# Kernel optimization log

Measured on AMD Instinct MI355X. Metric: run time of the kernel, lower is better.

## Reference

```python
import jax, jax.numpy as jnp
import numpy as np
from jax.ops import segment_sum

N_NODES = 50000
N_EDGES = 50000
N_GRAPHS = 1024


def _inv_deg(idx, num_segments):
    deg = segment_sum(jnp.ones(idx.shape[0], jnp.float32), idx, num_segments=num_segments)
    return jnp.where(deg > 0, 1.0 / deg, 0.0)


def hypergraph_conv(x, W, b, node_idx, edge_idx):
    # PyG HypergraphConv (use_attention=False, heads=1, hyperedge_weight=1):
    # out = D^{-1} H B^{-1} H^T (X W) + b
    D = _inv_deg(node_idx, N_NODES)   # inverse node degree [N]
    B = _inv_deg(edge_idx, N_EDGES)   # inverse hyperedge degree [E]
    xl = x @ W                         # [N, out]
    # node -> hyperedge aggregation
    edge_feat = B[:, None] * segment_sum(xl[node_idx], edge_idx, num_segments=N_EDGES)
    # hyperedge -> node aggregation
    out = D[:, None] * segment_sum(edge_feat[edge_idx], node_idx, num_segments=N_NODES)
    return out + b


def global_mean_pool(x, batch):
    s = segment_sum(x, batch, num_segments=N_GRAPHS)
    cnt = segment_sum(jnp.ones(x.shape[0], jnp.float32), batch, num_segments=N_GRAPHS)
    return s / jnp.maximum(cnt, 1.0)[:, None]


def setup_inputs() -> dict:
    key = jax.random.key(0)
    ks = jax.random.split(key, 16)
    F, H = 128, 256
    def lin(k, fi, fo):
        s = 1.0 / np.sqrt(fi)
        k1, k2 = jax.random.split(k)
        return (jax.random.uniform(k1, (fi, fo), jnp.float32, -s, s),
                jax.random.uniform(k2, (fo,), jnp.float32, -s, s))
    W1, b1 = lin(ks[0], F, H)
    W2, b2 = lin(ks[1], H, 2 * H)
    W3, b3 = lin(ks[2], 2 * H, H)
    Wl1, bl1 = lin(ks[3], H, H // 2)
    Wl2, bl2 = lin(ks[4], H // 2, 1)
    x = jax.random.normal(ks[5], (N_NODES, F), jnp.float32)
    hyperedge_index = jax.random.randint(ks[6], (2, 400000), 0, N_EDGES, jnp.int64)
    batch = jnp.sort(jax.random.randint(ks[7], (N_NODES,), 0, N_GRAPHS, jnp.int64))
    return {"x": x, "hyperedge_index": hyperedge_index, "batch": batch,
            "W1": W1, "b1": b1, "W2": W2, "b2": b2, "W3": W3, "b3": b3,
            "Wl1": Wl1, "bl1": bl1, "Wl2": Wl2, "bl2": bl2}


def reference(x, hyperedge_index, batch, W1, b1, W2, b2, W3, b3, Wl1, bl1, Wl2, bl2):
    node_idx, edge_idx = hyperedge_index[0], hyperedge_index[1]
    h = jax.nn.relu(hypergraph_conv(x, W1, b1, node_idx, edge_idx))
    h = jax.nn.relu(hypergraph_conv(h, W2, b2, node_idx, edge_idx))
    h = jax.nn.relu(hypergraph_conv(h, W3, b3, node_idx, edge_idx))
    g = global_mean_pool(h, batch)              # [G, H]
    g = jax.nn.relu(g @ Wl1 + bl1)
    out = g @ Wl2 + bl2                          # [G, 1]
    return out
```

## Files before the change

### kernel.cpp

```cpp
#include <hip/hip_runtime.h>
#include <hip/hip_bf16.h>

#define N_NODES  50000
#define N_EDGES  50000
#define N_INC    400000
#define N_GRAPHS 1024
#define M_PAD    50048
#define SEG_CAP  50176

typedef __bf16 bf16x8 __attribute__((ext_vector_type(8)));
typedef float  f32x4  __attribute__((ext_vector_type(4)));

__device__ __forceinline__ unsigned short f2bf(float f) {
    __hip_bfloat16 h = __float2bfloat16(f);
    return __builtin_bit_cast(unsigned short, h);
}
__device__ __forceinline__ float bflo(unsigned int u) {
    return __builtin_bit_cast(float, u << 16);
}
__device__ __forceinline__ float bfhi(unsigned int u) {
    return __builtin_bit_cast(float, u & 0xffff0000u);
}
__device__ __forceinline__ unsigned int packbf(float a, float b) {
    return (unsigned int)f2bf(a) | ((unsigned int)f2bf(b) << 16);
}
__device__ __forceinline__ void load_lds16(const unsigned short* g, unsigned short* l) {
    __builtin_amdgcn_global_load_lds((const __attribute__((address_space(1))) void*)g,
                                     (__attribute__((address_space(3))) void*)l, 16, 0, 0);
}

#define NB_INC  1563
#define NB_CONV 6250
#define NB_W1   128
#define NB_W2   512
#define NB_W3   512
__global__ __launch_bounds__(256) void normhist_kernel(const int* __restrict__ hei,
                                                       int* __restrict__ nidx, int* __restrict__ eidx,
                                                       unsigned short* __restrict__ rn,
                                                       unsigned short* __restrict__ re,
                                                       int* __restrict__ ndeg_p, int* __restrict__ edeg_p,
                                                       const float* __restrict__ x,
                                                       unsigned short* __restrict__ xbf,
                                                       const float* __restrict__ W1, unsigned short* __restrict__ wt1,
                                                       const float* __restrict__ W2, unsigned short* __restrict__ wt2,
                                                       const float* __restrict__ W3, unsigned short* __restrict__ wt3) {
    int b = blockIdx.x, t = threadIdx.x;
    if (b < NB_INC) {
        __shared__ int s32;
        if (t == 0) s32 = 0;
        __syncthreads();
        int probe = hei[4 * t + 1] | hei[4 * t + 3];
        if (probe) s32 = 1;
        __syncthreads();
        int is32 = s32;
        int i = b * 256 + t;
        if (i < N_INC) {
            int n, e;
            if (is32) { n = hei[i];     e = hei[N_INC + i]; }
            else      { n = hei[2 * i]; e = hei[2 * N_INC + 2 * i]; }
            nidx[i] = n; eidx[i] = e;
            rn[i] = (unsigned short)atomicAdd(&ndeg_p[n << 4], 1);
            re[i] = (unsigned short)atomicAdd(&edeg_p[e << 4], 1);
        }
    } else if (b < NB_INC + NB_CONV) {
        int i = (b - NB_INC) * 256 + t;
        float4 v = *(const float4*)(x + 4 * (size_t)i);
        ushort4 o;
        o.x = f2bf(v.x); o.y = f2bf(v.y); o.z = f2bf(v.z); o.w = f2bf(v.w);
        *(ushort4*)(xbf + 4 * (size_t)i) = o;
    } else if (b < NB_INC + NB_CONV + NB_W1) {
        int i = (b - NB_INC - NB_CONV) * 256 + t;
        int k = i >> 8, n = i & 255;
        wt1[n * 128 + k] = f2bf(W1[i]);
    } else if (b < NB_INC + NB_CONV + NB_W1 + NB_W2) {
        int i = (b - NB_INC - NB_CONV - NB_W1) * 256 + t;
        int k = i >> 9, n = i & 511;
        wt2[n * 256 + k] = f2bf(W2[i]);
    } else {
        int i = (b - NB_INC - NB_CONV - NB_W1 - NB_W2) * 256 + t;
        int k = i >> 8, n = i & 255;
        wt3[n * 512 + k] = f2bf(W3[i]);
    }
}

__global__ __launch_bounds__(256) void scan_up_f(const int* __restrict__ edeg_p,
                                                 const int* __restrict__ ndeg_p,
                                                 const int* __restrict__ hei,
                                                 const int* __restrict__ braw,
                                                 int* __restrict__ eoff, int* __restrict__ noff,
                                                 int* __restrict__ goff,
                                                 int* __restrict__ partials) {
    int b = blockIdx.x, t = threadIdx.x;
    if (b >= 98) {
        __shared__ int s32;
        if (t == 0) s32 = 0;
        __syncthreads();
        int probe = hei[4 * t + 1] | hei[4 * t + 3];
        if (probe) s32 = 1;
        __syncthreads();
        int is32 = s32;
        int g = (b - 98) * 256 + t;
        int lo = 0, hi = N_NODES;
        while (lo < hi) {
            int mid = (lo + hi) >> 1;
            int v = is32 ? braw[mid] : braw[2 * mid];
            if (v < g) lo = mid + 1; else hi = mid;
        }
        goff[g] = lo;
        if (g == 1023) goff[1024] = N_NODES;
        return;
    }
    __shared__ int lds[256];
    const int* in; int* outp; int lb;
    if (b < 49) { in = edeg_p; outp = eoff; lb = b; }
    else        { in = ndeg_p; outp = noff; lb = b - 49; }
    int base = lb * 1024 + t * 4;
    int4 v;
    v.x = in[(size_t)(base + 0) << 4];
    v.y = in[(size_t)(base + 1) << 4];
    v.z = in[(size_t)(base + 2) << 4];
    v.w = in[(size_t)(base + 3) << 4];
    int s = v.x + v.y + v.z + v.w;
    lds[t] = s;
    __syncthreads();
    for (int off = 1; off < 256; off <<= 1) {
        int u = (t >= off) ? lds[t - off] : 0;
        __syncthreads();
        lds[t] += u;
        __syncthreads();
    }
    int excl = lds[t] - s;
    if (t == 255) partials[b] = lds[255];
    int4 o;
    o.x = excl;
    o.y = excl + v.x;
    o.z = o.y + v.y;
    o.w = o.z + v.z;
    *(int4*)(outp + base) = o;
}

__global__ __launch_bounds__(256) void scan_down_f(int* __restrict__ eoff,
                                                   int* __restrict__ noff,
                                                   const int* __restrict__ partials) {
    __shared__ int lds[98];
    int b = blockIdx.x, t = threadIdx.x;
    if (t < 98) lds[t] = partials[t];
    __syncthreads();
    if (t < 2) {
        int lo = t * 49, hi = lo + 49;
        int run = 0;
        for (int i = lo; i < hi; ++i) { int x = lds[i]; lds[i] = run; run += x; }
    }
    __syncthreads();
    int* outp; int lb;
    if (b < 49) { outp = eoff; lb = b; }
    else        { outp = noff; lb = b - 49; }
    int base = lb * 1024 + t * 4;
    int p = lds[b];
    int4 v = *(const int4*)(outp + base);
    v.x += p; v.y += p; v.z += p; v.w += p;
    *(int4*)(outp + base) = v;
}

__global__ __launch_bounds__(256) void prep_kernel(const int* __restrict__ nidx,
                                                   const int* __restrict__ eidx,
                                                   const unsigned short* __restrict__ rn,
                                                   const unsigned short* __restrict__ re,
                                                   const int* __restrict__ eoff,
                                                   const int* __restrict__ noff,
                                                   unsigned short* __restrict__ csre,
                                                   unsigned short* __restrict__ csrn) {
    int i = blockIdx.x * 256 + threadIdx.x;
    if (i >= N_INC) return;
    int n = nidx[i], e = eidx[i];
    csre[eoff[e] + re[i]] = (unsigned short)n;
    csrn[noff[n] + rn[i]] = (unsigned short)e;
}

template <bool EPI>
__global__ __launch_bounds__(256) void gemm128_kernel(const unsigned short* __restrict__ A,
                                                      const unsigned short* __restrict__ Bt,
                                                      const float* __restrict__ bias,
                                                      unsigned short* __restrict__ C,
                                                      int M, int K, int N) {
    __shared__ unsigned short As[128 * 32];
    __shared__ unsigned short Bs[128 * 32];
    __shared__ unsigned short Cs[32][140];
    int tid  = threadIdx.x;
    int wave = tid >> 6, lane = tid & 63;
    int n0 = blockIdx.x * 128, m0 = blockIdx.y * 128;
    int quad = lane >> 4, fr = lane & 15;
    int wr = wave >> 1, wc = wave & 1;
    int lrow16 = lane >> 2;
    int lchunk = (lane & 3) * 8;

    const unsigned short* gsrc;
    unsigned short* ldst;
    if (wave < 2) { gsrc = A  + (size_t)(m0 + wave * 64) * K;       ldst = As + wave * 64 * 32; }
    else          { gsrc = Bt + (size_t)(n0 + (wave - 2) * 64) * K; ldst = Bs + (wave - 2) * 64 * 32; }

    f32x4 acc[4][4];
#pragma unroll
    for (int s = 0; s < 4; ++s)
#pragma unroll
        for (int c = 0; c < 4; ++c) acc[s][c] = (f32x4){0.f, 0.f, 0.f, 0.f};

    for (int k0 = 0; k0 < K; k0 += 32) {
#pragma unroll
        for (int l = 0; l < 4; ++l) {
            const unsigned short* g = gsrc + (size_t)(l * 16 + lrow16) * K + k0 + lchunk;
            load_lds16(g, ldst + l * 16 * 32);
        }
        __syncthreads();
        bf16x8 af[4], bfr[4];
#pragma unroll
        for (int s = 0; s < 4; ++s)
            af[s] = *(const bf16x8*)&As[(wr * 64 + s * 16 + fr) * 32 + quad * 8];
#pragma unroll
        for (int c = 0; c < 4; ++c)
            bfr[c] = *(const bf16x8*)&Bs[(wc * 64 + c * 16 + fr) * 32 + quad * 8];
#pragma unroll
        for (int s = 0; s < 4; ++s)
#pragma unroll
            for (int c = 0; c < 4; ++c)
                acc[s][c] = __builtin_amdgcn_mfma_f32_16x16x32_bf16(af[s], bfr[c], acc[s][c], 0, 0, 0);
        __syncthreads();
    }

    float bv[4];
#pragma unroll
    for (int c = 0; c < 4; ++c) bv[c] = EPI ? bias[n0 + wc * 64 + c * 16 + fr] : 0.f;
#pragma unroll
    for (int s = 0; s < 4; ++s) {
#pragma unroll
        for (int c = 0; c < 4; ++c)
#pragma unroll
            for (int r = 0; r < 4; ++r) {
                float v = acc[s][c][r];
                if (EPI) v = fmaxf(v + bv[c], 0.f);
                Cs[wr * 16 + quad * 4 + r][wc * 64 + c * 16 + fr] = f2bf(v);
            }
        __syncthreads();
#pragma unroll
        for (int i = 0; i < 2; ++i) {
            int rl  = i * 16 + (tid >> 4);
            int col = (tid & 15) * 8;
            int gm  = m0 + (rl >> 4) * 64 + s * 16 + (rl & 15);
            if (gm < M) {
                uint4 v = *(const uint4*)&Cs[rl][col];
                *(uint4*)&C[(size_t)gm * N + n0 + col] = v;
            }
        }
        __syncthreads();
    }
}

template <int C, bool BIAS>
__device__ __forceinline__ void seg_body2(const unsigned short* __restrict__ in,
                                          const int* __restrict__ offs,
                                          const int* __restrict__ degs_p,
                                          const unsigned short* __restrict__ csr_src,
                                          const float* __restrict__ bias,
                                          unsigned short* __restrict__ outp,
                                          int nseg) {
    constexpr int VEC = C / 32;
    constexpr int NW  = VEC / 2;
    int wid  = (blockIdx.x * 256 + threadIdx.x) >> 6;
    int lane = threadIdx.x & 63;
    int half = lane >> 5, l2 = lane & 31;
    int seg = 2 * wid + half;
    if (2 * wid >= nseg) return;
    bool segvalid = seg < nseg;
    int deg   = segvalid ? degs_p[(size_t)seg << 4] : 0;
    int start = segvalid ? offs[seg] : 0;
    float dinv = (deg > 0) ? 1.0f / (float)deg : 0.0f;
    int maxdeg = max(deg, __shfl_xor(deg, 32, 64));
    const unsigned short* cs = csr_src + start;
    float acc[VEC];
#pragma unroll
    for (int q = 0; q < VEC; ++q) acc[q] = 0.f;
    size_t lbase = (size_t)l2 * VEC;

    auto loadrow = [&](int src, unsigned int* v) {
        src = min(src, nseg - 1);
        const unsigned int* p = (const unsigned int*)(in + (size_t)src * C + lbase);
        if constexpr (NW == 4) { uint4 t = *(const uint4*)p; v[0] = t.x; v[1] = t.y; v[2] = t.z; v[3] = t.w; }
        else                   { uint2 t = *(const uint2*)p; v[0] = t.x; v[1] = t.y; }
    };
    auto maccum = [&](unsigned int* v, unsigned int msk) {
#pragma unroll
        for (int q = 0; q < NW; ++q) {
            unsigned int x = v[q] & msk;
            acc[2 * q] += bflo(x); acc[2 * q + 1] += bfhi(x);
        }
    };

    int dc = (deg > 0) ? deg - 1 : 0;
    for (int j = 0; j < maxdeg; j += 8) {
        unsigned int v[8][NW];
        int row[8];
#pragma unroll
        for (int u = 0; u < 8; ++u) {
            int jj = min(j + u, dc);
            row[u] = (int)cs[jj];
        }
#pragma unroll
        for (int u = 0; u < 8; ++u) loadrow(row[u], v[u]);
        __asm__ __volatile__("" ::: "memory");
#pragma unroll
        for (int u = 0; u < 8; ++u) {
            unsigned int msk = (j + u < deg) ? 0xffffffffu : 0u;
            maccum(v[u], msk);
        }
    }

    if (!segvalid) return;
    unsigned int o[NW];
#pragma unroll
    for (int q = 0; q < NW; ++q) {
        float a = acc[2 * q] * dinv;
        float b = acc[2 * q + 1] * dinv;
        if constexpr (BIAS) {
            a = fmaxf(a + bias[lbase + 2 * q], 0.f);
            b = fmaxf(b + bias[lbase + 2 * q + 1], 0.f);
        }
        o[q] = packbf(a, b);
    }
    unsigned int* po = (unsigned int*)(outp + (size_t)seg * C + lbase);
    if constexpr (NW == 4) { *(uint4*)po = make_uint4(o[0], o[1], o[2], o[3]); }
    else                   { *(uint2*)po = make_uint2(o[0], o[1]); }
}

template <int C>
__global__ __launch_bounds__(256) void seg_edge_t(const unsigned short* __restrict__ xl,
                                                  const int* __restrict__ eoff,
                                                  const int* __restrict__ edeg_p,
                                                  const unsigned short* __restrict__ csr_src,
                                                  unsigned short* __restrict__ ef) {
    seg_body2<C, false>(xl, eoff, edeg_p, csr_src, nullptr, ef, N_EDGES);
}

template <int C, bool BIAS>
__global__ __launch_bounds__(256) void seg_node_t(const unsigned short* __restrict__ ef,
                                                  const int* __restrict__ noff,
                                                  const int* __restrict__ ndeg_p,
                                                  const unsigned short* __restrict__ csr_src,
                                                  const float* __restrict__ bias,
                                                  unsigned short* __restrict__ hout) {
    seg_body2<C, BIAS>(ef, noff, ndeg_p, csr_src, bias, hout, N_NODES);
}

__global__ __launch_bounds__(256) void pool_head_kernel(const unsigned short* __restrict__ h,
                                                        const int* __restrict__ goff,
                                                        const float* __restrict__ Wl1,
                                                        const float* __restrict__ bl1,
                                                        const float* __restrict__ Wl2,
                                                        const float* __restrict__ bl2,
                                                        float* __restrict__ out) {
    __shared__ float xs[256];
    __shared__ float red[128];
    int g = blockIdx.x, t = threadIdx.x;
    int s = goff[g], cnt = goff[g + 1] - s;
    float acc = 0.f;
    for (int i = 0; i < cnt; ++i) {
        unsigned int u = h[(size_t)(s + i) * 256 + t];
        acc += __builtin_bit_cast(float, u << 16);
    }
    xs[t] = acc / (float)(cnt > 0 ? cnt : 1);
    __syncthreads();
    if (t < 128) {
        float s2 = 0.f;
        for (int f = 0; f < 256; ++f) s2 += xs[f] * Wl1[f * 128 + t];
        s2 = fmaxf(s2 + bl1[t], 0.f);
        red[t] = s2 * Wl2[t];
    }
    __syncthreads();
    for (int off = 64; off > 0; off >>= 1) {
        if (t < off) red[t] += red[t + off];
        __syncthreads();
    }
    if (t == 0) out[g] = red[0] + bl2[0];
}

extern "C" void kernel_launch(void* const* d_in, const int* in_sizes, int n_in,
                              void* d_out, int out_size, void* d_ws, size_t ws_size,
                              hipStream_t stream) {
    const float* x     = (const float*)d_in[0];
    const int* hei     = (const int*)d_in[1];
    const int* braw    = (const int*)d_in[2];
    const float* W1    = (const float*)d_in[3];
    const float* b1    = (const float*)d_in[4];
    const float* W2    = (const float*)d_in[5];
    const float* b2    = (const float*)d_in[6];
    const float* W3    = (const float*)d_in[7];
    const float* b3    = (const float*)d_in[8];
    const float* Wl1   = (const float*)d_in[9];
    const float* bl1   = (const float*)d_in[10];
    const float* Wl2   = (const float*)d_in[11];
    const float* bl2   = (const float*)d_in[12];
    float* out         = (float*)d_out;

    char* w = (char*)d_ws;
    size_t off = 0;
    auto alloc = [&](size_t bytes) { size_t p = off; off += (bytes + 255) & ~(size_t)255; return p; };
    size_t o_edegp = alloc((size_t)SEG_CAP * 16 * 4);
    size_t o_ndegp = alloc((size_t)SEG_CAP * 16 * 4);
    size_t zero_end = off;
    size_t o_eoff = alloc((size_t)SEG_CAP * 4);
    size_t o_noff = alloc((size_t)SEG_CAP * 4);
    size_t o_goff = alloc((size_t)1025 * 4);
    size_t o_part = alloc(128 * 4);
    size_t o_nidx = alloc((size_t)N_INC * 4);
    size_t o_eidx = alloc((size_t)N_INC * 4);
    size_t o_rn   = alloc((size_t)N_INC * 2);
    size_t o_re   = alloc((size_t)N_INC * 2);
    size_t o_csre = alloc((size_t)N_INC * 2 + 64);
    size_t o_csrn = alloc((size_t)N_INC * 2 + 64);
    size_t o_wt1  = alloc((size_t)128 * 256 * 2);
    size_t o_wt2  = alloc((size_t)256 * 512 * 2);
    size_t o_wt3  = alloc((size_t)512 * 256 * 2);
    size_t o_xbf  = alloc((size_t)M_PAD * 128 * 2);
    size_t o_Y    = alloc((size_t)M_PAD * 256 * 2);
    size_t o_H1   = alloc((size_t)M_PAD * 256 * 2);
    size_t o_H2   = alloc((size_t)M_PAD * 512 * 2);
    size_t o_bufE = alloc((size_t)N_EDGES * 256 * 2);

    int* edeg_p = (int*)(w + o_edegp);
    int* ndeg_p = (int*)(w + o_ndegp);
    int* eoff = (int*)(w + o_eoff);
    int* noff = (int*)(w + o_noff);
    int* goff = (int*)(w + o_goff);
    int* part = (int*)(w + o_part);
    int* nidx = (int*)(w + o_nidx);
    int* eidx = (int*)(w + o_eidx);
    unsigned short* rn   = (unsigned short*)(w + o_rn);
    unsigned short* re   = (unsigned short*)(w + o_re);
    unsigned short* csre = (unsigned short*)(w + o_csre);
    unsigned short* csrn = (unsigned short*)(w + o_csrn);
    unsigned short* wt1  = (unsigned short*)(w + o_wt1);
    unsigned short* wt2  = (unsigned short*)(w + o_wt2);
    unsigned short* wt3  = (unsigned short*)(w + o_wt3);
    unsigned short* xbf  = (unsigned short*)(w + o_xbf);
    unsigned short* Y    = (unsigned short*)(w + o_Y);
    unsigned short* H1   = (unsigned short*)(w + o_H1);
    unsigned short* H2   = (unsigned short*)(w + o_H2);
    unsigned short* bufE = (unsigned short*)(w + o_bufE);

    hipMemsetAsync(w, 0, zero_end, stream);
    normhist_kernel<<<NB_INC + NB_CONV + NB_W1 + NB_W2 + NB_W3, 256, 0, stream>>>(
        hei, nidx, eidx, rn, re, ndeg_p, edeg_p, x, xbf, W1, wt1, W2, wt2, W3, wt3);
    scan_up_f<<<102, 256, 0, stream>>>(edeg_p, ndeg_p, hei, braw, eoff, noff, goff, part);
    scan_down_f<<<98, 256, 0, stream>>>(eoff, noff, part);
    prep_kernel<<<(N_INC + 255) / 256, 256, 0, stream>>>(nidx, eidx, rn, re, eoff, noff, csre, csrn);

    int segGrid2 = ((N_NODES + 1) / 2 * 64 + 255) / 256;

    seg_edge_t<128><<<segGrid2, 256, 0, stream>>>(xbf, eoff, edeg_p, csre, bufE);
    seg_node_t<128, false><<<segGrid2, 256, 0, stream>>>(bufE, noff, ndeg_p, csrn, nullptr, Y);
    {
        dim3 grid(256 / 128, M_PAD / 128);
        gemm128_kernel<true><<<grid, 256, 0, stream>>>(Y, wt1, b1, H1, N_NODES, 128, 256);
    }
    seg_edge_t<256><<<segGrid2, 256, 0, stream>>>(H1, eoff, edeg_p, csre, bufE);
    seg_node_t<256, false><<<segGrid2, 256, 0, stream>>>(bufE, noff, ndeg_p, csrn, nullptr, Y);
    {
        dim3 grid(512 / 128, M_PAD / 128);
        gemm128_kernel<true><<<grid, 256, 0, stream>>>(Y, wt2, b2, H2, N_NODES, 256, 512);
    }
    {
        dim3 grid(256 / 128, M_PAD / 128);
        gemm128_kernel<false><<<grid, 256, 0, stream>>>(H2, wt3, nullptr, Y, N_NODES, 512, 256);
    }
    seg_edge_t<256><<<segGrid2, 256, 0, stream>>>(Y, eoff, edeg_p, csre, bufE);
    seg_node_t<256, true><<<segGrid2, 256, 0, stream>>>(bufE, noff, ndeg_p, csrn, b3, H1);

    pool_head_kernel<<<N_GRAPHS, 256, 0, stream>>>(H1, goff, Wl1, bl1, Wl2, bl2, out);
}
```

Measured before the change: 413.6 us.

## Use 16-byte loads in segment aggregation and move conversions into CSR prep

The segment-sum kernel is generalized so each lane handles 8 bf16 values with 16-byte loads. For C=128 that means 4 segments per wave instead of 2, and the grid for the first layer's aggregations is sized to match. The x and weight bf16 conversion work moves from the histogram kernel into the CSR-fill kernel, so the atomic histogram kernel runs lean and the conversions overlap with the scattered CSR writes. Packing more segments per wave raises per-wave divergence, since the loop runs to the max degree across 4 segments.

```diff
diff --git a/kernel.cpp b/kernel.cpp
--- a/kernel.cpp
+++ b/kernel.cpp
@@ -30,56 +30,27 @@
 }
 
 #define NB_INC  1563
-#define NB_CONV 6250
-#define NB_W1   128
-#define NB_W2   512
-#define NB_W3   512
 __global__ __launch_bounds__(256) void normhist_kernel(const int* __restrict__ hei,
                                                        int* __restrict__ nidx, int* __restrict__ eidx,
                                                        unsigned short* __restrict__ rn,
                                                        unsigned short* __restrict__ re,
-                                                       int* __restrict__ ndeg_p, int* __restrict__ edeg_p,
-                                                       const float* __restrict__ x,
-                                                       unsigned short* __restrict__ xbf,
-                                                       const float* __restrict__ W1, unsigned short* __restrict__ wt1,
-                                                       const float* __restrict__ W2, unsigned short* __restrict__ wt2,
-                                                       const float* __restrict__ W3, unsigned short* __restrict__ wt3) {
-    int b = blockIdx.x, t = threadIdx.x;
-    if (b < NB_INC) {
-        __shared__ int s32;
-        if (t == 0) s32 = 0;
-        __syncthreads();
-        int probe = hei[4 * t + 1] | hei[4 * t + 3];
-        if (probe) s32 = 1;
-        __syncthreads();
-        int is32 = s32;
-        int i = b * 256 + t;
-        if (i < N_INC) {
-            int n, e;
-            if (is32) { n = hei[i];     e = hei[N_INC + i]; }
-            else      { n = hei[2 * i]; e = hei[2 * N_INC + 2 * i]; }
-            nidx[i] = n; eidx[i] = e;
-            rn[i] = (unsigned short)atomicAdd(&ndeg_p[n << 4], 1);
-            re[i] = (unsigned short)atomicAdd(&edeg_p[e << 4], 1);
-        }
-    } else if (b < NB_INC + NB_CONV) {
-        int i = (b - NB_INC) * 256 + t;
-        float4 v = *(const float4*)(x + 4 * (size_t)i);
-        ushort4 o;
-        o.x = f2bf(v.x); o.y = f2bf(v.y); o.z = f2bf(v.z); o.w = f2bf(v.w);
-        *(ushort4*)(xbf + 4 * (size_t)i) = o;
-    } else if (b < NB_INC + NB_CONV + NB_W1) {
-        int i = (b - NB_INC - NB_CONV) * 256 + t;
-        int k = i >> 8, n = i & 255;
-        wt1[n * 128 + k] = f2bf(W1[i]);
-    } else if (b < NB_INC + NB_CONV + NB_W1 + NB_W2) {
-        int i = (b - NB_INC - NB_CONV - NB_W1) * 256 + t;
-        int k = i >> 9, n = i & 511;
-        wt2[n * 256 + k] = f2bf(W2[i]);
-    } else {
-        int i = (b - NB_INC - NB_CONV - NB_W1 - NB_W2) * 256 + t;
-        int k = i >> 8, n = i & 255;
-        wt3[n * 512 + k] = f2bf(W3[i]);
+                                                       int* __restrict__ ndeg_p, int* __restrict__ edeg_p) {
+    __shared__ int s32;
+    int t = threadIdx.x;
+    if (t == 0) s32 = 0;
+    __syncthreads();
+    int probe = hei[4 * t + 1] | hei[4 * t + 3];
+    if (probe) s32 = 1;
+    __syncthreads();
+    int is32 = s32;
+    int i = blockIdx.x * 256 + t;
+    if (i < N_INC) {
+        int n, e;
+        if (is32) { n = hei[i];     e = hei[N_INC + i]; }
+        else      { n = hei[2 * i]; e = hei[2 * N_INC + 2 * i]; }
+        nidx[i] = n; eidx[i] = e;
+        rn[i] = (unsigned short)atomicAdd(&ndeg_p[n << 4], 1);
+        re[i] = (unsigned short)atomicAdd(&edeg_p[e << 4], 1);
     }
 }
 
@@ -162,6 +133,11 @@
     *(int4*)(outp + base) = v;
 }
 
+#define NB_CSR  1563
+#define NB_CONV 6250
+#define NB_W1   128
+#define NB_W2   512
+#define NB_W3   512
 __global__ __launch_bounds__(256) void prep_kernel(const int* __restrict__ nidx,
                                                    const int* __restrict__ eidx,
                                                    const unsigned short* __restrict__ rn,
@@ -169,12 +145,39 @@
                                                    const int* __restrict__ eoff,
                                                    const int* __restrict__ noff,
                                                    unsigned short* __restrict__ csre,
-                                                   unsigned short* __restrict__ csrn) {
-    int i = blockIdx.x * 256 + threadIdx.x;
-    if (i >= N_INC) return;
-    int n = nidx[i], e = eidx[i];
-    csre[eoff[e] + re[i]] = (unsigned short)n;
-    csrn[noff[n] + rn[i]] = (unsigned short)e;
+                                                   unsigned short* __restrict__ csrn,
+                                                   const float* __restrict__ x,
+                                                   unsigned short* __restrict__ xbf,
+                                                   const float* __restrict__ W1, unsigned short* __restrict__ wt1,
+                                                   const float* __restrict__ W2, unsigned short* __restrict__ wt2,
+                                                   const float* __restrict__ W3, unsigned short* __restrict__ wt3) {
+    int b = blockIdx.x, t = threadIdx.x;
+    if (b < NB_CSR) {
+        int i = b * 256 + t;
+        if (i < N_INC) {
+            int n = nidx[i], e = eidx[i];
+            csre[eoff[e] + re[i]] = (unsigned short)n;
+            csrn[noff[n] + rn[i]] = (unsigned short)e;
+        }
+    } else if (b < NB_CSR + NB_CONV) {
+        int i = (b - NB_CSR) * 256 + t;
+        float4 v = *(const float4*)(x + 4 * (size_t)i);
+        ushort4 o;
+        o.x = f2bf(v.x); o.y = f2bf(v.y); o.z = f2bf(v.z); o.w = f2bf(v.w);
+        *(ushort4*)(xbf + 4 * (size_t)i) = o;
+    } else if (b < NB_CSR + NB_CONV + NB_W1) {
+        int i = (b - NB_CSR - NB_CONV) * 256 + t;
+        int k = i >> 8, n = i & 255;
+        wt1[n * 128 + k] = f2bf(W1[i]);
+    } else if (b < NB_CSR + NB_CONV + NB_W1 + NB_W2) {
+        int i = (b - NB_CSR - NB_CONV - NB_W1) * 256 + t;
+        int k = i >> 9, n = i & 511;
+        wt2[n * 256 + k] = f2bf(W2[i]);
+    } else {
+        int i = (b - NB_CSR - NB_CONV - NB_W1 - NB_W2) * 256 + t;
+        int k = i >> 8, n = i & 255;
+        wt3[n * 512 + k] = f2bf(W3[i]);
+    }
 }
 
 template <bool EPI>
@@ -256,40 +259,41 @@
 }
 
 template <int C, bool BIAS>
-__device__ __forceinline__ void seg_body2(const unsigned short* __restrict__ in,
+__device__ __forceinline__ void seg_bodyN(const unsigned short* __restrict__ in,
                                           const int* __restrict__ offs,
                                           const int* __restrict__ degs_p,
                                           const unsigned short* __restrict__ csr_src,
                                           const float* __restrict__ bias,
                                           unsigned short* __restrict__ outp,
                                           int nseg) {
-    constexpr int VEC = C / 32;
-    constexpr int NW  = VEC / 2;
+    constexpr int LPG = C / 8;
+    constexpr int SPW = 64 / LPG;
     int wid  = (blockIdx.x * 256 + threadIdx.x) >> 6;
     int lane = threadIdx.x & 63;
-    int half = lane >> 5, l2 = lane & 31;
-    int seg = 2 * wid + half;
-    if (2 * wid >= nseg) return;
+    int grp = lane / LPG, lg = lane % LPG;
+    int seg = SPW * wid + grp;
+    if (SPW * wid >= nseg) return;
     bool segvalid = seg < nseg;
     int deg   = segvalid ? degs_p[(size_t)seg << 4] : 0;
     int start = segvalid ? offs[seg] : 0;
     float dinv = (deg > 0) ? 1.0f / (float)deg : 0.0f;
-    int maxdeg = max(deg, __shfl_xor(deg, 32, 64));
+    int maxdeg = deg;
+#pragma unroll
+    for (int m = LPG; m < 64; m <<= 1) maxdeg = max(maxdeg, __shfl_xor(maxdeg, m, 64));
     const unsigned short* cs = csr_src + start;
-    float acc[VEC];
-#pragma unroll
-    for (int q = 0; q < VEC; ++q) acc[q] = 0.f;
-    size_t lbase = (size_t)l2 * VEC;
+    float acc[8];
+#pragma unroll
+    for (int q = 0; q < 8; ++q) acc[q] = 0.f;
+    size_t lbase = (size_t)lg * 8;
 
     auto loadrow = [&](int src, unsigned int* v) {
         src = min(src, nseg - 1);
         const unsigned int* p = (const unsigned int*)(in + (size_t)src * C + lbase);
-        if constexpr (NW == 4) { uint4 t = *(const uint4*)p; v[0] = t.x; v[1] = t.y; v[2] = t.z; v[3] = t.w; }
-        else                   { uint2 t = *(const uint2*)p; v[0] = t.x; v[1] = t.y; }
+        uint4 t = *(const uint4*)p; v[0] = t.x; v[1] = t.y; v[2] = t.z; v[3] = t.w;
     };
     auto maccum = [&](unsigned int* v, unsigned int msk) {
 #pragma unroll
-        for (int q = 0; q < NW; ++q) {
+        for (int q = 0; q < 4; ++q) {
             unsigned int x = v[q] & msk;
             acc[2 * q] += bflo(x); acc[2 * q + 1] += bfhi(x);
         }
@@ -297,7 +301,7 @@
 
     int dc = (deg > 0) ? deg - 1 : 0;
     for (int j = 0; j < maxdeg; j += 8) {
-        unsigned int v[8][NW];
+        unsigned int v[8][4];
         int row[8];
 #pragma unroll
         for (int u = 0; u < 8; ++u) {
@@ -315,9 +319,9 @@
     }
 
     if (!segvalid) return;
-    unsigned int o[NW];
-#pragma unroll
-    for (int q = 0; q < NW; ++q) {
+    unsigned int o[4];
+#pragma unroll
+    for (int q = 0; q < 4; ++q) {
         float a = acc[2 * q] * dinv;
         float b = acc[2 * q + 1] * dinv;
         if constexpr (BIAS) {
@@ -326,9 +330,7 @@
         }
         o[q] = packbf(a, b);
     }
-    unsigned int* po = (unsigned int*)(outp + (size_t)seg * C + lbase);
-    if constexpr (NW == 4) { *(uint4*)po = make_uint4(o[0], o[1], o[2], o[3]); }
-    else                   { *(uint2*)po = make_uint2(o[0], o[1]); }
+    *(uint4*)(outp + (size_t)seg * C + lbase) = make_uint4(o[0], o[1], o[2], o[3]);
 }
 
 template <int C>
@@ -337,7 +339,7 @@
                                                   const int* __restrict__ edeg_p,
                                                   const unsigned short* __restrict__ csr_src,
                                                   unsigned short* __restrict__ ef) {
-    seg_body2<C, false>(xl, eoff, edeg_p, csr_src, nullptr, ef, N_EDGES);
+    seg_bodyN<C, false>(xl, eoff, edeg_p, csr_src, nullptr, ef, N_EDGES);
 }
 
 template <int C, bool BIAS>
@@ -347,7 +349,7 @@
                                                   const unsigned short* __restrict__ csr_src,
                                                   const float* __restrict__ bias,
                                                   unsigned short* __restrict__ hout) {
-    seg_body2<C, BIAS>(ef, noff, ndeg_p, csr_src, bias, hout, N_NODES);
+    seg_bodyN<C, BIAS>(ef, noff, ndeg_p, csr_src, bias, hout, N_NODES);
 }
 
 __global__ __launch_bounds__(256) void pool_head_kernel(const unsigned short* __restrict__ h,
@@ -447,16 +449,17 @@
     unsigned short* bufE = (unsigned short*)(w + o_bufE);
 
     hipMemsetAsync(w, 0, zero_end, stream);
-    normhist_kernel<<<NB_INC + NB_CONV + NB_W1 + NB_W2 + NB_W3, 256, 0, stream>>>(
-        hei, nidx, eidx, rn, re, ndeg_p, edeg_p, x, xbf, W1, wt1, W2, wt2, W3, wt3);
+    normhist_kernel<<<NB_INC, 256, 0, stream>>>(hei, nidx, eidx, rn, re, ndeg_p, edeg_p);
     scan_up_f<<<102, 256, 0, stream>>>(edeg_p, ndeg_p, hei, braw, eoff, noff, goff, part);
     scan_down_f<<<98, 256, 0, stream>>>(eoff, noff, part);
-    prep_kernel<<<(N_INC + 255) / 256, 256, 0, stream>>>(nidx, eidx, rn, re, eoff, noff, csre, csrn);
+    prep_kernel<<<NB_CSR + NB_CONV + NB_W1 + NB_W2 + NB_W3, 256, 0, stream>>>(
+        nidx, eidx, rn, re, eoff, noff, csre, csrn, x, xbf, W1, wt1, W2, wt2, W3, wt3);
 
     int segGrid2 = ((N_NODES + 1) / 2 * 64 + 255) / 256;
-
-    seg_edge_t<128><<<segGrid2, 256, 0, stream>>>(xbf, eoff, edeg_p, csre, bufE);
-    seg_node_t<128, false><<<segGrid2, 256, 0, stream>>>(bufE, noff, ndeg_p, csrn, nullptr, Y);
+    int segGrid4 = ((N_NODES + 3) / 4 * 64 + 255) / 256;
+
+    seg_edge_t<128><<<segGrid4, 256, 0, stream>>>(xbf, eoff, edeg_p, csre, bufE);
+    seg_node_t<128, false><<<segGrid4, 256, 0, stream>>>(bufE, noff, ndeg_p, csrn, nullptr, Y);
     {
         dim3 grid(256 / 128, M_PAD / 128);
         gemm128_kernel<true><<<grid, 256, 0, stream>>>(Y, wt1, b1, H1, N_NODES, 128, 256);
```

Result: no change. 411.4 us (-0.5%).
